# Performance work log

Measured on AMD Instinct MI355X. Metric: run time of the kernel, lower is better.

Reference implementation:

```python
import jax, jax.numpy as jnp
import numpy as np

G, NPG, EPG = 1024, 126, 450      # graphs, nodes/graph, edges/graph
N, E, F = G * NPG, G * EPG, 126
EPS = 1e-5


def setup_inputs() -> dict:
    key = jax.random.key(0)
    ks = jax.random.split(key, 30)
    nrm = lambda k, s, sc=0.05: jax.random.normal(k, s, jnp.float32) * sc
    # graph data: random intra-graph connectivity (offsets keep edges inside each graph)
    src = jax.random.randint(ks[0], (E,), 0, NPG, jnp.int32)
    dst = jax.random.randint(ks[1], (E,), 0, NPG, jnp.int32)
    off = jnp.repeat(jnp.arange(G, dtype=jnp.int32) * NPG, EPG)
    inp = {
        "x": jax.random.normal(ks[2], (N, 5), jnp.float32),
        "edge_index": jnp.stack([src + off, dst + off]),            # [2,E] int32
        "edge_attr": jax.random.randint(ks[3], (E,), 0, 10, jnp.int32),
        "batch": jnp.repeat(jnp.arange(G, dtype=jnp.int32), NPG),   # [N]
        "deg_hist": jnp.array([0, 100, 3000, 50000, 20000], jnp.int32),  # length-5 degree histogram
        # parameters (4 PNA layers stacked on leading axis)
        "emb1_w": nrm(ks[4], (5, F)), "emb1_b": nrm(ks[5], (F,)),
        "edge_tab": nrm(ks[6], (10, 50)),
        "enc_w": nrm(ks[7], (4, 50, F)), "enc_b": nrm(ks[8], (4, F)),
        "pre_w": nrm(ks[9], (4, 3 * F, F)), "pre_b": nrm(ks[10], (4, F)),
        "post_w": nrm(ks[11], (4, 13 * F, F)), "post_b": nrm(ks[12], (4, F)),
        "lin_w": nrm(ks[13], (4, F, F)), "lin_b": nrm(ks[14], (4, F)),
        "bn_g": jnp.ones((4, F), jnp.float32), "bn_b": jnp.zeros((4, F), jnp.float32),
        "mlp_w1": nrm(ks[15], (F, 100)), "mlp_b1": nrm(ks[16], (100,)),
        "mlp_w2": nrm(ks[17], (100, 50)), "mlp_b2": nrm(ks[18], (50,)),
        "mlp_w3": nrm(ks[19], (50, 25)), "mlp_b3": nrm(ks[20], (25,)),
        "mlp_w4": nrm(ks[21], (25, 1)), "mlp_b4": nrm(ks[22], (1,)),
    }
    return inp


def _finite(a):
    return jnp.where(jnp.isfinite(a), a, 0.0)


def reference(x, edge_index, edge_attr, batch, deg_hist,
              emb1_w, emb1_b, edge_tab,
              enc_w, enc_b, pre_w, pre_b, post_w, post_b, lin_w, lin_b,
              bn_g, bn_b,
              mlp_w1, mlp_b1, mlp_w2, mlp_b2, mlp_w3, mlp_b3, mlp_w4, mlp_b4):
    src, dst = edge_index[0], edge_index[1]          # x_j = x[src], x_i = x[dst]
    h = x @ emb1_w + emb1_b                          # [N,126] node embedding
    ea_emb = edge_tab[edge_attr]                     # [E,50] edge embedding

    # PNA degree statistics (from the init-time degree histogram, as in PyG PNAConv)
    dh = deg_hist.astype(jnp.float32)
    bins = jnp.arange(dh.shape[0], dtype=jnp.float32)
    avg_log = jnp.sum(dh * jnp.log(bins + 1.0)) / jnp.sum(dh)

    cnt = jax.ops.segment_sum(jnp.ones((E,), jnp.float32), dst, N)  # in-degree per node
    inv_cnt = (1.0 / jnp.maximum(cnt, 1.0))[:, None]
    d = jnp.clip(cnt, 1.0)[:, None]
    amp = jnp.log(d + 1.0) / avg_log                  # amplification scaler
    att = avg_log / jnp.log(d + 1.0)                  # attenuation scaler

    for l in range(4):
        # message: pre_nn(cat[x_i, x_j, edge_encoder(e)])
        ea = ea_emb @ enc_w[l] + enc_b[l]             # [E,126]
        m = jnp.concatenate([h[dst], h[src], ea], -1) @ pre_w[l] + pre_b[l]  # [E,126]
        # aggregators: mean, min, max, std
        mean = jax.ops.segment_sum(m, dst, N) * inv_cnt
        meansq = jax.ops.segment_sum(m * m, dst, N) * inv_cnt
        std = jnp.sqrt(jax.nn.relu(meansq - mean * mean) + EPS)
        mn = _finite(jax.ops.segment_min(m, dst, N))
        mx = _finite(jax.ops.segment_max(m, dst, N))
        agg = jnp.concatenate([mean, mn, mx, std], -1)               # [N,504]
        agg = jnp.concatenate([agg, agg * amp, agg * att], -1)       # [N,1512] scalers
        # update: post_nn(cat[x, agg]) then lin
        out = jnp.concatenate([h, agg], -1) @ post_w[l] + post_b[l]  # [N,126]
        out = out @ lin_w[l] + lin_b[l]
        # BatchNorm (training-mode batch stats over nodes) + ReLU
        mu = out.mean(0)
        var = out.var(0)
        h = jax.nn.relu(bn_g[l] * (out - mu) / jnp.sqrt(var + EPS) + bn_b[l])

    pooled = jax.ops.segment_sum(h, batch, G)         # global_add_pool -> [G,126]
    z = jax.nn.relu(pooled @ mlp_w1 + mlp_b1)
    z = jax.nn.relu(z @ mlp_w2 + mlp_b2)
    z = jax.nn.relu(z @ mlp_w3 + mlp_b3)
    return z @ mlp_w4 + mlp_b4                        # [G,1]
```

## Files before the change

kernel.cpp:

```cpp
#include <hip/hip_runtime.h>
#include <math.h>

#define G_    1024
#define NPG   126
#define EPG   450
#define NN    (G_*NPG)
#define EE    (G_*EPG)
#define F_    126
#define EPSV  1e-5f

#define KS_POST 20
#define SEGB_SZ (KS_POST*8*64*8)
#define SMALLB_SZ (4*8*64*8)

typedef unsigned short u16;
typedef unsigned int   u32;
typedef __attribute__((ext_vector_type(8))) short bf8v;
typedef __attribute__((ext_vector_type(4))) float f4v;

union U4 { bf8v v; u32 a[4]; };

__device__ __forceinline__ u16 f2b(float f) {
    u32 u = __float_as_uint(f);
    u += 0x7FFFu + ((u >> 16) & 1u);
    return (u16)(u >> 16);
}
__device__ __forceinline__ float b2f(u16 s) { return __uint_as_float(((u32)s) << 16); }
__device__ __forceinline__ float b2f_lo(u32 u) { return __uint_as_float(u << 16); }
__device__ __forceinline__ float b2f_hi(u32 u) { return __uint_as_float(u & 0xFFFF0000u); }

__device__ __forceinline__ bf8v bn_load(const u16* __restrict__ p,
                                        const float* __restrict__ coef, int k0) {
    U4 r; r.v = *(const bf8v*)p;
    if (!coef) return r.v;
    f4v s0 = *(const f4v*)(coef + k0);
    f4v s1 = *(const f4v*)(coef + k0 + 4);
    f4v h0 = *(const f4v*)(coef + 128 + k0);
    f4v h1 = *(const f4v*)(coef + 128 + k0 + 4);
    float v[8];
#pragma unroll
    for (int i = 0; i < 4; ++i) { v[2 * i] = b2f_lo(r.a[i]); v[2 * i + 1] = b2f_hi(r.a[i]); }
    v[0] = fmaxf(v[0] * s0[0] + h0[0], 0.f); v[1] = fmaxf(v[1] * s0[1] + h0[1], 0.f);
    v[2] = fmaxf(v[2] * s0[2] + h0[2], 0.f); v[3] = fmaxf(v[3] * s0[3] + h0[3], 0.f);
    v[4] = fmaxf(v[4] * s1[0] + h1[0], 0.f); v[5] = fmaxf(v[5] * s1[1] + h1[1], 0.f);
    v[6] = fmaxf(v[6] * s1[2] + h1[2], 0.f); v[7] = fmaxf(v[7] * s1[3] + h1[3], 0.f);
    U4 o;
#pragma unroll
    for (int i = 0; i < 4; ++i) o.a[i] = (u32)f2b(v[2 * i]) | ((u32)f2b(v[2 * i + 1]) << 16);
    return o.v;
}

__global__ void k_embed(const float* __restrict__ x, const float* __restrict__ w,
                        const float* __restrict__ b, u16* __restrict__ hb) {
    int idx = (blockIdx.x * 256 + threadIdx.x) * 8;
    if (idx >= NN * 128) return;
    int n = idx >> 7, f0 = idx & 127;
    float xr[5];
#pragma unroll
    for (int c = 0; c < 5; ++c) xr[c] = x[n * 5 + c];
    float v[8];
#pragma unroll
    for (int j = 0; j < 8; ++j) {
        int f = f0 + j;
        float s = 0.f;
        if (f < F_) {
            s = b[f];
#pragma unroll
            for (int c = 0; c < 5; ++c) s += xr[c] * w[c * F_ + f];
        }
        v[j] = s;
    }
    U4 o;
#pragma unroll
    for (int i = 0; i < 4; ++i) o.a[i] = (u32)f2b(v[2 * i]) | ((u32)f2b(v[2 * i + 1]) << 16);
    *(bf8v*)(hb + idx) = o.v;
}

__global__ void k_build_csr(const int* __restrict__ src, const int* __restrict__ dst,
                            const int* __restrict__ attr,
                            int* __restrict__ deg, int* __restrict__ rstart,
                            int* __restrict__ epack) {
    int g = blockIdx.x;
    __shared__ int scnt[NPG];
    __shared__ int spos[NPG];
    int t = threadIdx.x;
    for (int j = t; j < NPG; j += blockDim.x) scnt[j] = 0;
    __syncthreads();
    int e0 = g * EPG;
    for (int i = t; i < EPG; i += blockDim.x) {
        int dl = dst[e0 + i] - g * NPG;
        atomicAdd(&scnt[dl], 1);
    }
    __syncthreads();
    if (t == 0) {
        int run = 0;
        for (int j = 0; j < NPG; ++j) { spos[j] = run; run += scnt[j]; }
    }
    __syncthreads();
    for (int j = t; j < NPG; j += blockDim.x) {
        deg[g * NPG + j]    = scnt[j];
        rstart[g * NPG + j] = e0 + spos[j];
    }
    __syncthreads();
    for (int j = t; j < NPG; j += blockDim.x) scnt[j] = 0;
    __syncthreads();
    for (int i = t; i < EPG; i += blockDim.x) {
        int e  = e0 + i;
        int dl = dst[e] - g * NPG;
        int p  = atomicAdd(&scnt[dl], 1);
        epack[e0 + spos[dl] + p] = (src[e] - g * NPG) | (attr[e] << 8);
    }
}

__global__ void k_build_etab(const float* __restrict__ edge_tab, const float* __restrict__ enc_w,
                             const float* __restrict__ enc_b, const float* __restrict__ pre_w,
                             const float* __restrict__ pre_b, float* __restrict__ etab) {
    int l = blockIdx.x / 10, a = blockIdx.x % 10;
    __shared__ float tmp[F_];
    int t = threadIdx.x;
    if (t < F_) {
        float s = enc_b[l * F_ + t];
        for (int c = 0; c < 50; ++c) s += edge_tab[a * 50 + c] * enc_w[(l * 50 + c) * F_ + t];
        tmp[t] = s;
    }
    __syncthreads();
    if (t < F_) {
        float s = pre_b[l * F_ + t];
        for (int j = 0; j < F_; ++j) s += tmp[j] * pre_w[((size_t)l * 378 + 252 + j) * F_ + t];
        etab[(l * 10 + a) * F_ + t] = s;
    }
}

__global__ void k_fold_T(const float* __restrict__ pre_w, const float* __restrict__ post_w,
                         float* __restrict__ Tbuf) {
    int k = blockIdx.x;
    int y = blockIdx.y;
    int l = y / 3, seg = y % 3;
    int c = threadIdx.x;
    __shared__ float wi[128];
    wi[c] = (k < F_ && c < F_) ? pre_w[((size_t)l * 378 + k) * F_ + c] : 0.f;
    __syncthreads();
    float s = 0.f;
    if (k < F_ && c < F_) {
        const float* pw = post_w + (size_t)l * 1638 * F_;
        if (seg == 0) s = pw[(size_t)k * F_ + c];
        int base = 126 + seg * 504;
        for (int f = 0; f < F_; ++f) {
            float bs = pw[(size_t)(base + f) * F_ + c]
                     + pw[(size_t)(base + 126 + f) * F_ + c]
                     + pw[(size_t)(base + 252 + f) * F_ + c];
            s += wi[f] * bs;
        }
    }
    Tbuf[((size_t)y * 128 + k) * 128 + c] = s;
}

__global__ void k_fold_Wc(const float* __restrict__ Tbuf, const float* __restrict__ post_w,
                          const int* __restrict__ deg_hist, float* __restrict__ WcBuf) {
    int idx = blockIdx.x * 256 + threadIdx.x;
    if (idx >= 4 * 128 * 128) return;
    int l = idx >> 14, k = (idx >> 7) & 127, c = idx & 127;
    float dsum = 0.f, dsl = 0.f;
#pragma unroll
    for (int b = 0; b < 5; ++b) {
        float dh = (float)deg_hist[b];
        dsum += dh; dsl += dh * logf((float)b + 1.f);
    }
    float avgl = dsl / dsum;
    float l2 = logf(2.f);
    float amp0 = l2 / avgl, att0 = avgl / l2;
    float t1 = Tbuf[((size_t)(l * 3 + 0) * 128 + k) * 128 + c];
    float t2 = Tbuf[((size_t)(l * 3 + 1) * 128 + k) * 128 + c];
    float t3 = Tbuf[((size_t)(l * 3 + 2) * 128 + k) * 128 + c];
    float b0 = (k < F_ && c < F_) ? post_w[((size_t)l * 1638 + k) * F_ + c] : 0.f;
    WcBuf[((size_t)l * 128 + k) * 128 + c] = -((t1 - b0) + amp0 * t2 + att0 * t3);
}

__global__ void k_prep_B128(const float* __restrict__ pre_w, const float* __restrict__ lin_w,
                            const float* __restrict__ WcBuf,
                            u16* __restrict__ wjB, u16* __restrict__ linB,
                            u16* __restrict__ wcB) {
    int idx = blockIdx.x * 256 + threadIdx.x;
    int y = blockIdx.y;
    int l = y & 3, ty = y >> 2;
    int j = idx & 7, lane = (idx >> 3) & 63, pnl = (idx >> 9) & 7, ks = idx >> 12;
    int k = ks * 32 + (lane >> 4) * 8 + j;
    int c = pnl * 16 + (lane & 15);
    float v;
    if (ty == 2) {
        v = WcBuf[((size_t)l * 128 + k) * 128 + c];
    } else {
        const float* W = (ty == 0) ? pre_w + ((size_t)l * 378 + 126) * F_
                                   : lin_w + (size_t)l * F_ * F_;
        v = (k < F_ && c < F_) ? W[(size_t)k * F_ + c] : 0.f;
    }
    u16* out = ((ty == 0) ? wjB : (ty == 1) ? linB : wcB) + (size_t)l * SMALLB_SZ;
    out[idx] = f2b(v);
}

__global__ void k_prep_Bpost(const float* __restrict__ post_w, const float* __restrict__ Tbuf,
                             u16* __restrict__ postB) {
    int idx = blockIdx.x * 256 + threadIdx.x;
    if (idx >= SEGB_SZ) return;
    int y = blockIdx.y;
    int l = y / 3, seg = y % 3;
    int j = idx & 7, lane = (idx >> 3) & 63, pnl = (idx >> 9) & 7, ks = idx >> 12;
    int c  = pnl * 16 + (lane & 15);
    int kk = (lane >> 4) * 8 + j;
    float val = 0.f;
    if (ks < 4) {
        int k = ks * 32 + kk;
        val = Tbuf[((size_t)y * 128 + k) * 128 + c];
    } else {
        int kv = (ks - 4) * 32 + kk;
        int f = kv >> 2, t = kv & 3;
        if (f < F_ && c < F_)
            val = post_w[((size_t)l * 1638 + 126 + seg * 504 + t * 126 + f) * F_ + c];
    }
    postB[(size_t)y * SEGB_SZ + idx] = f2b(val);
}

__global__ __launch_bounds__(256) void k_psgemm(
        const u16* __restrict__ A0, const float* __restrict__ coef,
        const u16* __restrict__ Bv0, const u16* __restrict__ Bv1,
        u16* __restrict__ C0, u16* __restrict__ C1) {
    const u16* Bv = blockIdx.y ? Bv1 : Bv0;
    u16* C = blockIdx.y ? C1 : C0;
    int lane = threadIdx.x & 63, wid = threadIdx.x >> 6;
    int gq = lane >> 4, r15 = lane & 15;
    int wr = (wid >> 1) * 32, wc = (wid & 1) * 64;
    const u16* bp = Bv + ((size_t)(wc >> 4) * 64 + lane) * 8;
    bf8v bfr[16];
#pragma unroll
    for (int ks = 0; ks < 4; ++ks)
#pragma unroll
        for (int fc = 0; fc < 4; ++fc)
            bfr[ks * 4 + fc] = *(const bf8v*)(bp + (size_t)ks * 4096 + fc * 512);

#pragma unroll
    for (int t = 0; t < 4; ++t) {
        size_t rbase = ((size_t)blockIdx.x * 4 + t) * 64;
        size_t row0 = rbase + wr + r15;
        const u16* a0p = A0 + row0 * 128 + gq * 8;
        const u16* a1p = a0p + 16 * 128;
        f4v acc[2][4];
#pragma unroll
        for (int i = 0; i < 2; ++i)
#pragma unroll
            for (int j = 0; j < 4; ++j) acc[i][j] = (f4v){0.f, 0.f, 0.f, 0.f};
#pragma unroll
        for (int ks = 0; ks < 4; ++ks) {
            int k0 = ks * 32 + gq * 8;
            bf8v a0 = bn_load(a0p + ks * 32, coef, k0);
            bf8v a1 = bn_load(a1p + ks * 32, coef, k0);
#pragma unroll
            for (int fc = 0; fc < 4; ++fc) {
                acc[0][fc] = __builtin_amdgcn_mfma_f32_16x16x32_bf16(a0, bfr[ks * 4 + fc], acc[0][fc], 0, 0, 0);
                acc[1][fc] = __builtin_amdgcn_mfma_f32_16x16x32_bf16(a1, bfr[ks * 4 + fc], acc[1][fc], 0, 0, 0);
            }
        }
        int erow = (int)rbase + wr + gq * 4;
        int ecol = wc + r15;
#pragma unroll
        for (int fc = 0; fc < 4; ++fc) {
            int col = ecol + fc * 16;
#pragma unroll
            for (int fr = 0; fr < 2; ++fr)
#pragma unroll
                for (int r = 0; r < 4; ++r) {
                    size_t row = erow + fr * 16 + r;
                    C[row * 128 + col] = (col < F_) ? f2b(acc[fr][fc][r]) : (u16)0;
                }
        }
    }
}

__global__ __launch_bounds__(512) void k_agg2(
        const u16* __restrict__ Psc,
        const float* __restrict__ etab_l,
        const int* __restrict__ deg, const int* __restrict__ rstart,
        const int* __restrict__ epack,
        u16* __restrict__ aggc, int g0) {
    __shared__ u32  PsL[126 * 65];
    __shared__ float etLo[10 * 64];
    __shared__ float etHi[10 * 64];
    __shared__ u32  epL[EPG];
    __shared__ int  degL[NPG];
    __shared__ int  rlL[NPG];
    int gg = g0 + blockIdx.x;
    int tid = threadIdx.x;
    const u16* psrow = Psc + (size_t)blockIdx.x * NPG * 128;
    for (int i = tid; i < NPG * 16; i += 512) {
        int r = i >> 4, q = i & 15;
        U4 u; u.v = *(const bf8v*)(psrow + (size_t)r * 128 + q * 8);
        u32* dp = &PsL[r * 65 + q * 4];
        dp[0] = u.a[0]; dp[1] = u.a[1]; dp[2] = u.a[2]; dp[3] = u.a[3];
    }
    for (int i = tid; i < 640; i += 512) {
        int a = i >> 6, ln = i & 63;
        int f = 2 * ln;
        etLo[i] = (f < F_) ? etab_l[a * F_ + f] : 0.f;
        etHi[i] = (f + 1 < F_) ? etab_l[a * F_ + f + 1] : 0.f;
    }
    for (int e = tid; e < EPG; e += 512) epL[e] = (u32)epack[(size_t)gg * EPG + e];
    if (tid < NPG) {
        degL[tid] = deg[(size_t)gg * NPG + tid];
        rlL[tid]  = rstart[(size_t)gg * NPG + tid] - gg * EPG;
    }
    __syncthreads();

    int lane = tid & 63, wid = tid >> 6;
    for (int nd = wid; nd < NPG; nd += 8) {
        int dg = degL[nd], rl = rlL[nd];
        float s0 = 0.f, q0 = 0.f, s1 = 0.f, q1 = 0.f;
        float n0 = 3.4e38f, x0 = -3.4e38f, n1 = 3.4e38f, x1 = -3.4e38f;
        for (int e = 0; e < dg; ++e) {
            u32 pk = epL[rl + e];
            int sN = pk & 255, at = pk >> 8;
            u32 pv = PsL[sN * 65 + lane];
            float v0 = b2f_lo(pv) + etLo[at * 64 + lane];
            float v1 = b2f_hi(pv) + etHi[at * 64 + lane];
            s0 += v0; q0 += v0 * v0; n0 = fminf(n0, v0); x0 = fmaxf(x0, v0);
            s1 += v1; q1 += v1 * v1; n1 = fminf(n1, v1); x1 = fmaxf(x1, v1);
        }
        float m0, m1, d0, d1;
        if (dg == 0) {
            m0 = m1 = 0.f; n0 = x0 = n1 = x1 = 0.f;
            d0 = d1 = 0.0031622776601683794f;
        } else {
            float ic = 1.f / (float)dg;
            m0 = s0 * ic; m1 = s1 * ic;
            d0 = sqrtf(fmaxf(q0 * ic - m0 * m0, 0.f) + EPSV);
            d1 = sqrtf(fmaxf(q1 * ic - m1 * m1, 0.f) + EPSV);
        }
        U4 o;
        o.a[0] = (u32)f2b(m0) | ((u32)f2b(n0) << 16);
        o.a[1] = (u32)f2b(x0) | ((u32)f2b(d0) << 16);
        o.a[2] = (u32)f2b(m1) | ((u32)f2b(n1) << 16);
        o.a[3] = (u32)f2b(x1) | ((u32)f2b(d1) << 16);
        *(bf8v*)(aggc + ((size_t)blockIdx.x * NPG + nd) * 512 + lane * 8) = o.v;
    }
}

__global__ __launch_bounds__(512, 4) void k_post2(
        const u16* __restrict__ hA, const float* __restrict__ coef,
        const u16* __restrict__ aggc, const u16* __restrict__ corr,
        const int* __restrict__ degc, const int* __restrict__ deg_hist,
        const u16* __restrict__ postB_l, const float* __restrict__ bias,
        u16* __restrict__ outC) {
    int lane = threadIdx.x & 63, wid = threadIdx.x >> 6;
    int gq = lane >> 4, r15 = lane & 15;
    int wr = (wid >> 2) * 32;
    int wc = (wid & 3) * 32;
    const u16* bp = postB_l + ((size_t)(wc >> 4) * 64 + lane) * 8;
    float dsum = 0.f, dsl = 0.f;
#pragma unroll
    for (int b = 0; b < 5; ++b) {
        float dh = (float)deg_hist[b];
        dsum += dh; dsl += dh * logf((float)b + 1.f);
    }
    float avgl = dsl / dsum;

    size_t rbase = (size_t)blockIdx.x * 64;
    size_t row0 = rbase + wr + r15;
    const u16* h0 = hA + row0 * 128 + gq * 8;
    const u16* h1 = h0 + 16 * 128;
    const u16* g0p = aggc + row0 * 512 + gq * 8;
    const u16* g1p = g0p + 16 * 512;
    f4v acc[3][2][2];
#pragma unroll
    for (int s = 0; s < 3; ++s)
#pragma unroll
        for (int i = 0; i < 2; ++i)
#pragma unroll
            for (int j = 0; j < 2; ++j) acc[s][i][j] = (f4v){0.f, 0.f, 0.f, 0.f};

#pragma unroll
    for (int ks = 0; ks < 4; ++ks) {
        int k0 = ks * 32 + gq * 8;
        bf8v a0 = bn_load(h0 + ks * 32, coef, k0);
        bf8v a1 = bn_load(h1 + ks * 32, coef, k0);
        const u16* bk = bp + (size_t)ks * 4096;
#pragma unroll
        for (int seg = 0; seg < 3; ++seg) {
            const u16* bs = bk + (size_t)seg * SEGB_SZ;
#pragma unroll
            for (int fc = 0; fc < 2; ++fc) {
                bf8v bb = *(const bf8v*)(bs + fc * 512);
                acc[seg][0][fc] = __builtin_amdgcn_mfma_f32_16x16x32_bf16(a0, bb, acc[seg][0][fc], 0, 0, 0);
                acc[seg][1][fc] = __builtin_amdgcn_mfma_f32_16x16x32_bf16(a1, bb, acc[seg][1][fc], 0, 0, 0);
            }
        }
    }
#pragma unroll 4
    for (int ks = 0; ks < 16; ++ks) {
        bf8v a0 = *(const bf8v*)(g0p + ks * 32);
        bf8v a1 = *(const bf8v*)(g1p + ks * 32);
        const u16* bk = bp + (size_t)(4 + ks) * 4096;
#pragma unroll
        for (int seg = 0; seg < 3; ++seg) {
            const u16* bs = bk + (size_t)seg * SEGB_SZ;
#pragma unroll
            for (int fc = 0; fc < 2; ++fc) {
                bf8v bb = *(const bf8v*)(bs + fc * 512);
                acc[seg][0][fc] = __builtin_amdgcn_mfma_f32_16x16x32_bf16(a0, bb, acc[seg][0][fc], 0, 0, 0);
                acc[seg][1][fc] = __builtin_amdgcn_mfma_f32_16x16x32_bf16(a1, bb, acc[seg][1][fc], 0, 0, 0);
            }
        }
    }
    int erow = (int)rbase + wr + gq * 4;
    int ecol = wc + r15;
#pragma unroll
    for (int fr = 0; fr < 2; ++fr) {
#pragma unroll
        for (int rr = 0; rr < 4; ++rr) {
            size_t row = erow + fr * 16 + rr;
            int d = degc[row];
            float la = logf(fmaxf((float)d, 1.f) + 1.f);
            float am = la / avgl, at = avgl / la;
            bool isz = (d == 0);
#pragma unroll
            for (int fc = 0; fc < 2; ++fc) {
                int col = ecol + fc * 16;
                float val = acc[0][fr][fc][rr] + am * acc[1][fr][fc][rr]
                          + at * acc[2][fr][fc][rr];
                u16 ov = 0;
                if (col < F_) {
                    val += bias[col];
                    if (isz) val += b2f(corr[row * 128 + col]);
                    ov = f2b(val);
                }
                outC[row * 128 + col] = ov;
            }
        }
    }
}

__global__ __launch_bounds__(256) void k_lin(
        const u16* __restrict__ A0, const u16* __restrict__ Bv,
        const float* __restrict__ bias, float* __restrict__ bns,
        u16* __restrict__ C) {
    __shared__ float ldsS[128];
    __shared__ float ldsQ[128];
    int tid = threadIdx.x;
    if (tid < 128) { ldsS[tid] = 0.f; ldsQ[tid] = 0.f; }
    __syncthreads();
    int lane = tid & 63, wid = tid >> 6;
    int gq = lane >> 4, r15 = lane & 15;
    int wr = (wid >> 1) * 32, wc = (wid & 1) * 64;
    const u16* bp = Bv + ((size_t)(wc >> 4) * 64 + lane) * 8;
    bf8v bfr[16];
#pragma unroll
    for (int ks = 0; ks < 4; ++ks)
#pragma unroll
        for (int fc = 0; fc < 4; ++fc)
            bfr[ks * 4 + fc] = *(const bf8v*)(bp + (size_t)ks * 4096 + fc * 512);
    int ecol = wc + r15;
    float bv4[4], sc4[4] = {0.f, 0.f, 0.f, 0.f}, sq4[4] = {0.f, 0.f, 0.f, 0.f};
#pragma unroll
    for (int fc = 0; fc < 4; ++fc) {
        int col = ecol + fc * 16;
        bv4[fc] = (col < F_) ? bias[col] : 0.f;
    }

#pragma unroll
    for (int t = 0; t < 4; ++t) {
        size_t rbase = ((size_t)blockIdx.x * 4 + t) * 64;
        size_t row0 = rbase + wr + r15;
        const u16* a0p = A0 + row0 * 128 + gq * 8;
        const u16* a1p = a0p + 16 * 128;
        f4v acc[2][4];
#pragma unroll
        for (int i = 0; i < 2; ++i)
#pragma unroll
            for (int j = 0; j < 4; ++j) acc[i][j] = (f4v){0.f, 0.f, 0.f, 0.f};
#pragma unroll
        for (int ks = 0; ks < 4; ++ks) {
            bf8v a0 = *(const bf8v*)(a0p + ks * 32);
            bf8v a1 = *(const bf8v*)(a1p + ks * 32);
#pragma unroll
            for (int fc = 0; fc < 4; ++fc) {
                acc[0][fc] = __builtin_amdgcn_mfma_f32_16x16x32_bf16(a0, bfr[ks * 4 + fc], acc[0][fc], 0, 0, 0);
                acc[1][fc] = __builtin_amdgcn_mfma_f32_16x16x32_bf16(a1, bfr[ks * 4 + fc], acc[1][fc], 0, 0, 0);
            }
        }
        int erow = (int)rbase + wr + gq * 4;
#pragma unroll
        for (int fc = 0; fc < 4; ++fc) {
            int col = ecol + fc * 16;
#pragma unroll
            for (int fr = 0; fr < 2; ++fr)
#pragma unroll
                for (int r = 0; r < 4; ++r) {
                    size_t row = erow + fr * 16 + r;
                    float val = acc[fr][fc][r] + bv4[fc];
                    sc4[fc] += val; sq4[fc] += val * val;
                    C[row * 128 + col] = (col < F_) ? f2b(val) : (u16)0;
                }
        }
    }
#pragma unroll
    for (int fc = 0; fc < 4; ++fc) {
        int col = ecol + fc * 16;
        atomicAdd(&ldsS[col], sc4[fc]);
        atomicAdd(&ldsQ[col], sq4[fc]);
    }
    __syncthreads();
    if (tid < 128) {
        atomicAdd(&bns[tid], ldsS[tid]);
        atomicAdd(&bns[128 + tid], ldsQ[tid]);
    }
}

__global__ void k_bn_coef(const float* __restrict__ bns, const float* __restrict__ g,
                          const float* __restrict__ b, float* __restrict__ coef) {
    int f = threadIdx.x;
    float sc = 0.f, sh = 0.f;
    if (f < F_) {
        float mu  = bns[f] * (1.f / NN);
        float var = bns[128 + f] * (1.f / NN) - mu * mu;
        float r = rsqrtf(fmaxf(var, 0.f) + EPSV);
        sc = g[f] * r;
        sh = b[f] - mu * sc;
    }
    coef[f] = sc;
    coef[128 + f] = sh;
}

__global__ __launch_bounds__(256) void k_pool_mlp(const u16* __restrict__ hb,
        const float* __restrict__ coef,
        const float* __restrict__ w1, const float* __restrict__ b1,
        const float* __restrict__ w2, const float* __restrict__ b2,
        const float* __restrict__ w3, const float* __restrict__ b3,
        const float* __restrict__ w4, const float* __restrict__ b4,
        float* __restrict__ out) {
    int gg = blockIdx.x;
    __shared__ float lsum[16][128];
    __shared__ float p[128];
    __shared__ float z1[100];
    __shared__ float z2[50];
    __shared__ float z3[25];
    int t = threadIdx.x;
    int cg = t & 15, rs = t >> 4;
    float sc[8], sh[8];
#pragma unroll
    for (int j = 0; j < 8; ++j) { sc[j] = coef[cg * 8 + j]; sh[j] = coef[128 + cg * 8 + j]; }
    const u16* hbase = hb + (size_t)gg * NPG * 128 + cg * 8;
    float a8[8] = {};
    for (int r = rs; r < NPG; r += 16) {
        U4 u;
        u.v = *(const bf8v*)(hbase + (size_t)r * 128);
        float v[8];
#pragma unroll
        for (int i = 0; i < 4; ++i) { v[2 * i] = b2f_lo(u.a[i]); v[2 * i + 1] = b2f_hi(u.a[i]); }
#pragma unroll
        for (int j = 0; j < 8; ++j) a8[j] += fmaxf(v[j] * sc[j] + sh[j], 0.f);
    }
#pragma unroll
    for (int j = 0; j < 8; ++j) lsum[rs][cg * 8 + j] = a8[j];
    __syncthreads();
    if (t < 128) {
        float s = 0.f;
#pragma unroll
        for (int k = 0; k < 16; ++k) s += lsum[k][t];
        p[t] = s;
    }
    __syncthreads();
    if (t < 100) {
        float s = b1[t];
        for (int c = 0; c < F_; ++c) s += p[c] * w1[c * 100 + t];
        z1[t] = fmaxf(s, 0.f);
    }
    __syncthreads();
    if (t < 50) {
        float s = b2[t];
        for (int c = 0; c < 100; ++c) s += z1[c] * w2[c * 50 + t];
        z2[t] = fmaxf(s, 0.f);
    }
    __syncthreads();
    if (t < 25) {
        float s = b3[t];
        for (int c = 0; c < 50; ++c) s += z2[c] * w3[c * 25 + t];
        z3[t] = fmaxf(s, 0.f);
    }
    __syncthreads();
    if (t == 0) {
        float s = b4[0];
        for (int c = 0; c < 25; ++c) s += z3[c] * w4[c];
        out[gg] = s;
    }
}

extern "C" void kernel_launch(void* const* d_in, const int* in_sizes, int n_in,
                              void* d_out, int out_size, void* d_ws, size_t ws_size,
                              hipStream_t stream) {
    const float* x        = (const float*)d_in[0];
    const int*   ei       = (const int*)d_in[1];
    const int*   src      = ei;
    const int*   dst      = ei + EE;
    const int*   eattr    = (const int*)d_in[2];
    const int*   deg_hist = (const int*)d_in[4];
    const float* emb1_w = (const float*)d_in[5];
    const float* emb1_b = (const float*)d_in[6];
    const float* edge_tab = (const float*)d_in[7];
    const float* enc_w  = (const float*)d_in[8];
    const float* enc_b  = (const float*)d_in[9];
    const float* pre_w  = (const float*)d_in[10];
    const float* pre_b  = (const float*)d_in[11];
    const float* post_w = (const float*)d_in[12];
    const float* post_b = (const float*)d_in[13];
    const float* lin_w  = (const float*)d_in[14];
    const float* lin_b  = (const float*)d_in[15];
    const float* bn_g   = (const float*)d_in[16];
    const float* bn_b   = (const float*)d_in[17];
    const float* w1 = (const float*)d_in[18];
    const float* b1 = (const float*)d_in[19];
    const float* w2 = (const float*)d_in[20];
    const float* b2 = (const float*)d_in[21];
    const float* w3 = (const float*)d_in[22];
    const float* b3 = (const float*)d_in[23];
    const float* w4 = (const float*)d_in[24];
    const float* b4 = (const float*)d_in[25];
    float* out = (float*)d_out;

    size_t fixedB = 0;
    {
        fixedB += 3 * ((size_t)NN * 128 * 2 + 256);
        fixedB += 4 * 10 * F_ * 4 + 256;
        fixedB += (size_t)12 * 128 * 128 * 4 + 256;
        fixedB += (size_t)4 * 128 * 128 * 4 + 256;
        fixedB += 2 * (4 * 256 * 4 + 256);
        fixedB += 2 * ((size_t)NN * 4 + 256);
        fixedB += (size_t)EE * 4 + 256;
        fixedB += 3 * ((size_t)4 * SMALLB_SZ * 2 + 256);
        fixedB += (size_t)12 * SEGB_SZ * 2 + 256;
    }
    int nch = (ws_size >= fixedB + (size_t)NN * 512 * 2 + 256) ? 1 : 2;
    int GCH_ = G_ / nch;
    size_t CH_ = (size_t)NN / nch;

    char* base = (char*)d_ws;
    size_t o = 0;
    auto alloc = [&](size_t bytes) { char* r = base + o; o = (o + bytes + 255) & ~(size_t)255; return r; };
    u16*  hb    = (u16*)  alloc((size_t)NN * 128 * 2);
    u16*  Ps    = (u16*)  alloc((size_t)NN * 128 * 2);
    u16*  outA  = (u16*)  alloc((size_t)NN * 128 * 2);
    u16*  aggb  = (u16*)  alloc(CH_ * 512 * 2);
    float* etab = (float*)alloc(4 * 10 * F_ * 4);
    float* Tbuf = (float*)alloc((size_t)12 * 128 * 128 * 4);
    float* WcBuf= (float*)alloc((size_t)4 * 128 * 128 * 4);
    float* bns  = (float*)alloc(4 * 256 * 4);
    float* coef = (float*)alloc(4 * 256 * 4);
    int*  deg    = (int*)alloc((size_t)NN * 4);
    int*  rstart = (int*)alloc((size_t)NN * 4);
    int*  epack  = (int*)alloc((size_t)EE * 4);
    u16*  wjB   = (u16*)alloc((size_t)4 * SMALLB_SZ * 2);
    u16*  linB  = (u16*)alloc((size_t)4 * SMALLB_SZ * 2);
    u16*  wcB   = (u16*)alloc((size_t)4 * SMALLB_SZ * 2);
    u16*  postB = (u16*)alloc((size_t)12 * SEGB_SZ * 2);
    u16*  corr  = outA;

    hipMemsetAsync(bns, 0, 4 * 256 * 4, stream);
    k_embed<<<(NN * 128 / 8 + 255) / 256, 256, 0, stream>>>(x, emb1_w, emb1_b, hb);
    k_build_csr<<<G_, 128, 0, stream>>>(src, dst, eattr, deg, rstart, epack);
    k_build_etab<<<40, 128, 0, stream>>>(edge_tab, enc_w, enc_b, pre_w, pre_b, etab);
    k_fold_T<<<dim3(128, 12), 128, 0, stream>>>(pre_w, post_w, Tbuf);
    k_fold_Wc<<<(4 * 128 * 128 + 255) / 256, 256, 0, stream>>>(Tbuf, post_w, deg_hist, WcBuf);
    k_prep_B128<<<dim3(SMALLB_SZ / 256, 12), 256, 0, stream>>>(pre_w, lin_w, WcBuf, wjB, linB, wcB);
    k_prep_Bpost<<<dim3((SEGB_SZ + 255) / 256, 12), 256, 0, stream>>>(post_w, Tbuf, postB);

    for (int l = 0; l < 4; ++l) {
        const float* coefL = (l == 0) ? nullptr : coef + (size_t)(l - 1) * 256;
        k_psgemm<<<dim3(NN / 256, 2), 256, 0, stream>>>(
            hb, coefL, wjB + (size_t)l * SMALLB_SZ, wcB + (size_t)l * SMALLB_SZ, Ps, corr);
        for (int c = 0; c < nch; ++c) {
            int g0 = c * GCH_;
            size_t r0 = (size_t)g0 * NPG;
            k_agg2<<<GCH_, 512, 0, stream>>>(Ps + r0 * 128, etab + l * 10 * F_,
                                             deg, rstart, epack, aggb, g0);
            k_post2<<<(int)(CH_ / 64), 512, 0, stream>>>(
                hb + r0 * 128, coefL, aggb, corr + r0 * 128,
                deg + r0, deg_hist,
                postB + (size_t)(l * 3) * SEGB_SZ, post_b + l * F_, outA + r0 * 128);
        }
        k_lin<<<NN / 256, 256, 0, stream>>>(outA, linB + (size_t)l * SMALLB_SZ,
                                            lin_b + l * F_, bns + (size_t)l * 256, hb);
        k_bn_coef<<<1, 128, 0, stream>>>(bns + (size_t)l * 256, bn_g + l * F_, bn_b + l * F_,
                                         coef + (size_t)l * 256);
    }

    k_pool_mlp<<<G_, 256, 0, stream>>>(hb, coef + 3 * 256,
                                       w1, b1, w2, b2, w3, b3, w4, b4, out);
}
```

Baseline: 1.205 ms.

## Switch post GEMM to 32x32x16 MFMA with prefetched B and precomputed degree scalers

Rewrites the post-aggregation GEMM kernel to use 32x32x16 bf16 MFMA tiles. Each of 4 waves now owns a 32-column slice across 64 rows, and the B fragments for the next k-step are software-prefetched. The post weight layout is repacked to match. Per-node amplification and attenuation scalers are precomputed once in a new kernel instead of evaluating logs in every block's epilogue. The block size drops from 512 to 256 threads, which gives fewer waves per block and a different register budget.

```diff
diff --git a/kernel.cpp b/kernel.cpp
--- a/kernel.cpp
+++ b/kernel.cpp
@@ -9,14 +9,15 @@
 #define F_    126
 #define EPSV  1e-5f
 
-#define KS_POST 20
-#define SEGB_SZ (KS_POST*8*64*8)
+#define KS32  40
+#define SEGB_SZ (KS32*4*64*8)
 #define SMALLB_SZ (4*8*64*8)
 
 typedef unsigned short u16;
 typedef unsigned int   u32;
 typedef __attribute__((ext_vector_type(8))) short bf8v;
 typedef __attribute__((ext_vector_type(4))) float f4v;
+typedef __attribute__((ext_vector_type(16))) float f16v;
 
 union U4 { bf8v v; u32 a[4]; };
 
@@ -110,6 +111,24 @@
         int p  = atomicAdd(&scnt[dl], 1);
         epack[e0 + spos[dl] + p] = (src[e] - g * NPG) | (attr[e] << 8);
     }
+}
+
+__global__ void k_node_scalars(const int* __restrict__ deg, const int* __restrict__ deg_hist,
+                               float* __restrict__ ampv, float* __restrict__ attv) {
+    int n = blockIdx.x * blockDim.x + threadIdx.x;
+    if (n >= NN) return;
+    float sum = 0.f, sl = 0.f;
+#pragma unroll
+    for (int b = 0; b < 5; ++b) {
+        float dh = (float)deg_hist[b];
+        sum += dh;
+        sl  += dh * logf((float)b + 1.f);
+    }
+    float avg_log = sl / sum;
+    float cm = fmaxf((float)deg[n], 1.f);
+    float la = logf(cm + 1.f);
+    ampv[n] = la / avg_log;
+    attv[n] = avg_log / la;
 }
 
 __global__ void k_build_etab(const float* __restrict__ edge_tab, const float* __restrict__ enc_w,
@@ -204,15 +223,14 @@
     if (idx >= SEGB_SZ) return;
     int y = blockIdx.y;
     int l = y / 3, seg = y % 3;
-    int j = idx & 7, lane = (idx >> 3) & 63, pnl = (idx >> 9) & 7, ks = idx >> 12;
-    int c  = pnl * 16 + (lane & 15);
-    int kk = (lane >> 4) * 8 + j;
+    int j = idx & 7, lane = (idx >> 3) & 63, cg = (idx >> 9) & 3, ks = idx >> 11;
+    int c  = cg * 32 + (lane & 31);
+    int vk = ks * 16 + (lane >> 5) * 8 + j;
     float val = 0.f;
-    if (ks < 4) {
-        int k = ks * 32 + kk;
-        val = Tbuf[((size_t)y * 128 + k) * 128 + c];
+    if (vk < 128) {
+        val = Tbuf[((size_t)y * 128 + vk) * 128 + c];
     } else {
-        int kv = (ks - 4) * 32 + kk;
+        int kv = vk - 128;
         int f = kv >> 2, t = kv & 3;
         if (f < F_ && c < F_)
             val = post_w[((size_t)l * 1638 + 126 + seg * 504 + t * 126 + f) * F_ + c];
@@ -342,96 +360,80 @@
     }
 }
 
-__global__ __launch_bounds__(512, 4) void k_post2(
+__global__ __launch_bounds__(256) void k_post2(
         const u16* __restrict__ hA, const float* __restrict__ coef,
         const u16* __restrict__ aggc, const u16* __restrict__ corr,
-        const int* __restrict__ degc, const int* __restrict__ deg_hist,
+        const int* __restrict__ degc,
+        const float* __restrict__ ampc, const float* __restrict__ attc,
         const u16* __restrict__ postB_l, const float* __restrict__ bias,
         u16* __restrict__ outC) {
-    int lane = threadIdx.x & 63, wid = threadIdx.x >> 6;
-    int gq = lane >> 4, r15 = lane & 15;
-    int wr = (wid >> 2) * 32;
-    int wc = (wid & 3) * 32;
-    const u16* bp = postB_l + ((size_t)(wc >> 4) * 64 + lane) * 8;
-    float dsum = 0.f, dsl = 0.f;
-#pragma unroll
-    for (int b = 0; b < 5; ++b) {
-        float dh = (float)deg_hist[b];
-        dsum += dh; dsl += dh * logf((float)b + 1.f);
-    }
-    float avgl = dsl / dsum;
-
+    int lane = threadIdx.x & 63, cgw = threadIdx.x >> 6;
+    int r31 = lane & 31, kg = lane >> 5;
     size_t rbase = (size_t)blockIdx.x * 64;
-    size_t row0 = rbase + wr + r15;
-    const u16* h0 = hA + row0 * 128 + gq * 8;
-    const u16* h1 = h0 + 16 * 128;
-    const u16* g0p = aggc + row0 * 512 + gq * 8;
-    const u16* g1p = g0p + 16 * 512;
-    f4v acc[3][2][2];
+    const u16* h0 = hA + (rbase + r31) * 128 + kg * 8;
+    const u16* h1 = h0 + 32 * 128;
+    const u16* g0 = aggc + (rbase + r31) * 512 + kg * 8;
+    const u16* g1 = g0 + 32 * 512;
+    const u16* bp = postB_l + ((size_t)cgw * 64 + lane) * 8;
+
+    f16v acc[3][2];
 #pragma unroll
     for (int s = 0; s < 3; ++s)
 #pragma unroll
         for (int i = 0; i < 2; ++i)
 #pragma unroll
-            for (int j = 0; j < 2; ++j) acc[s][i][j] = (f4v){0.f, 0.f, 0.f, 0.f};
-
-#pragma unroll
-    for (int ks = 0; ks < 4; ++ks) {
-        int k0 = ks * 32 + gq * 8;
-        bf8v a0 = bn_load(h0 + ks * 32, coef, k0);
-        bf8v a1 = bn_load(h1 + ks * 32, coef, k0);
-        const u16* bk = bp + (size_t)ks * 4096;
-#pragma unroll
-        for (int seg = 0; seg < 3; ++seg) {
-            const u16* bs = bk + (size_t)seg * SEGB_SZ;
-#pragma unroll
-            for (int fc = 0; fc < 2; ++fc) {
-                bf8v bb = *(const bf8v*)(bs + fc * 512);
-                acc[seg][0][fc] = __builtin_amdgcn_mfma_f32_16x16x32_bf16(a0, bb, acc[seg][0][fc], 0, 0, 0);
-                acc[seg][1][fc] = __builtin_amdgcn_mfma_f32_16x16x32_bf16(a1, bb, acc[seg][1][fc], 0, 0, 0);
+            for (int r = 0; r < 16; ++r) acc[s][i][r] = 0.f;
+
+    bf8v bc0 = *(const bf8v*)(bp);
+    bf8v bc1 = *(const bf8v*)(bp + SEGB_SZ);
+    bf8v bc2 = *(const bf8v*)(bp + 2 * SEGB_SZ);
+
+#pragma unroll 4
+    for (int ks = 0; ks < KS32; ++ks) {
+        bf8v bn0, bn1, bn2;
+        if (ks < KS32 - 1) {
+            const u16* bn = bp + (size_t)(ks + 1) * 2048;
+            bn0 = *(const bf8v*)(bn);
+            bn1 = *(const bf8v*)(bn + SEGB_SZ);
+            bn2 = *(const bf8v*)(bn + 2 * SEGB_SZ);
+        }
+        bf8v a0, a1;
+        if (ks < 8) {
+            int k0 = ks * 16 + kg * 8;
+            a0 = bn_load(h0 + ks * 16, coef, k0);
+            a1 = bn_load(h1 + ks * 16, coef, k0);
+        } else {
+            int off = (ks - 8) * 16;
+            a0 = *(const bf8v*)(g0 + off);
+            a1 = *(const bf8v*)(g1 + off);
+        }
+        acc[0][0] = __builtin_amdgcn_mfma_f32_32x32x16_bf16(a0, bc0, acc[0][0], 0, 0, 0);
+        acc[0][1] = __builtin_amdgcn_mfma_f32_32x32x16_bf16(a1, bc0, acc[0][1], 0, 0, 0);
+        acc[1][0] = __builtin_amdgcn_mfma_f32_32x32x16_bf16(a0, bc1, acc[1][0], 0, 0, 0);
+        acc[1][1] = __builtin_amdgcn_mfma_f32_32x32x16_bf16(a1, bc1, acc[1][1], 0, 0, 0);
+        acc[2][0] = __builtin_amdgcn_mfma_f32_32x32x16_bf16(a0, bc2, acc[2][0], 0, 0, 0);
+        acc[2][1] = __builtin_amdgcn_mfma_f32_32x32x16_bf16(a1, bc2, acc[2][1], 0, 0, 0);
+        bc0 = bn0; bc1 = bn1; bc2 = bn2;
+    }
+
+    int ecol = cgw * 32 + r31;
+    float bv = (ecol < F_) ? bias[ecol] : 0.f;
+#pragma unroll
+    for (int rf = 0; rf < 2; ++rf) {
+#pragma unroll
+        for (int r = 0; r < 16; ++r) {
+            int rowl = rf * 32 + (r & 3) + 8 * (r >> 2) + 4 * kg;
+            size_t row = rbase + rowl;
+            float am = ampc[row], at = attc[row];
+            bool isz = (degc[row] == 0);
+            float val = acc[0][rf][r] + am * acc[1][rf][r] + at * acc[2][rf][r];
+            u16 ov = 0;
+            if (ecol < F_) {
+                val += bv;
+                if (isz) val += b2f(corr[row * 128 + ecol]);
+                ov = f2b(val);
             }
-        }
-    }
-#pragma unroll 4
-    for (int ks = 0; ks < 16; ++ks) {
-        bf8v a0 = *(const bf8v*)(g0p + ks * 32);
-        bf8v a1 = *(const bf8v*)(g1p + ks * 32);
-        const u16* bk = bp + (size_t)(4 + ks) * 4096;
-#pragma unroll
-        for (int seg = 0; seg < 3; ++seg) {
-            const u16* bs = bk + (size_t)seg * SEGB_SZ;
-#pragma unroll
-            for (int fc = 0; fc < 2; ++fc) {
-                bf8v bb = *(const bf8v*)(bs + fc * 512);
-                acc[seg][0][fc] = __builtin_amdgcn_mfma_f32_16x16x32_bf16(a0, bb, acc[seg][0][fc], 0, 0, 0);
-                acc[seg][1][fc] = __builtin_amdgcn_mfma_f32_16x16x32_bf16(a1, bb, acc[seg][1][fc], 0, 0, 0);
-            }
-        }
-    }
-    int erow = (int)rbase + wr + gq * 4;
-    int ecol = wc + r15;
-#pragma unroll
-    for (int fr = 0; fr < 2; ++fr) {
-#pragma unroll
-        for (int rr = 0; rr < 4; ++rr) {
-            size_t row = erow + fr * 16 + rr;
-            int d = degc[row];
-            float la = logf(fmaxf((float)d, 1.f) + 1.f);
-            float am = la / avgl, at = avgl / la;
-            bool isz = (d == 0);
-#pragma unroll
-            for (int fc = 0; fc < 2; ++fc) {
-                int col = ecol + fc * 16;
-                float val = acc[0][fr][fc][rr] + am * acc[1][fr][fc][rr]
-                          + at * acc[2][fr][fc][rr];
-                u16 ov = 0;
-                if (col < F_) {
-                    val += bias[col];
-                    if (isz) val += b2f(corr[row * 128 + col]);
-                    ov = f2b(val);
-                }
-                outC[row * 128 + col] = ov;
-            }
+            outC[row * 128 + ecol] = ov;
         }
     }
 }
@@ -631,6 +633,7 @@
         fixedB += (size_t)4 * 128 * 128 * 4 + 256;
         fixedB += 2 * (4 * 256 * 4 + 256);
         fixedB += 2 * ((size_t)NN * 4 + 256);
+        fixedB += 2 * ((size_t)NN * 4 + 256);
         fixedB += (size_t)EE * 4 + 256;
         fixedB += 3 * ((size_t)4 * SMALLB_SZ * 2 + 256);
         fixedB += (size_t)12 * SEGB_SZ * 2 + 256;
@@ -653,6 +656,8 @@
     float* coef = (float*)alloc(4 * 256 * 4);
     int*  deg    = (int*)alloc((size_t)NN * 4);
     int*  rstart = (int*)alloc((size_t)NN * 4);
+    float* ampv  = (float*)alloc((size_t)NN * 4);
+    float* attv  = (float*)alloc((size_t)NN * 4);
     int*  epack  = (int*)alloc((size_t)EE * 4);
     u16*  wjB   = (u16*)alloc((size_t)4 * SMALLB_SZ * 2);
     u16*  linB  = (u16*)alloc((size_t)4 * SMALLB_SZ * 2);
@@ -663,6 +668,7 @@
     hipMemsetAsync(bns, 0, 4 * 256 * 4, stream);
     k_embed<<<(NN * 128 / 8 + 255) / 256, 256, 0, stream>>>(x, emb1_w, emb1_b, hb);
     k_build_csr<<<G_, 128, 0, stream>>>(src, dst, eattr, deg, rstart, epack);
+    k_node_scalars<<<(NN + 255) / 256, 256, 0, stream>>>(deg, deg_hist, ampv, attv);
     k_build_etab<<<40, 128, 0, stream>>>(edge_tab, enc_w, enc_b, pre_w, pre_b, etab);
     k_fold_T<<<dim3(128, 12), 128, 0, stream>>>(pre_w, post_w, Tbuf);
     k_fold_Wc<<<(4 * 128 * 128 + 255) / 256, 256, 0, stream>>>(Tbuf, post_w, deg_hist, WcBuf);
@@ -678,9 +684,9 @@
             size_t r0 = (size_t)g0 * NPG;
             k_agg2<<<GCH_, 512, 0, stream>>>(Ps + r0 * 128, etab + l * 10 * F_,
                                              deg, rstart, epack, aggb, g0);
-            k_post2<<<(int)(CH_ / 64), 512, 0, stream>>>(
+            k_post2<<<(int)(CH_ / 64), 256, 0, stream>>>(
                 hb + r0 * 128, coefL, aggb, corr + r0 * 128,
-                deg + r0, deg_hist,
+                deg + r0, ampv + r0, attv + r0,
                 postB + (size_t)(l * 3) * SEGB_SZ, post_b + l * F_, outA + r0 * 128);
         }
         k_lin<<<NN / 256, 256, 0, stream>>>(outA, linB + (size_t)l * SMALLB_SZ,
```

Measured after the change: 1.174 ms. 2.6% less time.
